# Kernel tuning notes

Measured on AMD Instinct MI355X. Metric: run time of the kernel, lower is better.

Reference implementation:

```python
import jax, jax.numpy as jnp
import numpy as np

NUM_USERS = 100000
NUM_ITEMS = 50000
EMB_DIM = 128
N_EDGES = 1600000
BATCH = 16384
L_USER = (0, 1, 2)


def setup_inputs() -> dict:
    key = jax.random.key(0)
    k1, k2, k3, k4, k5, k6 = jax.random.split(key, 6)
    users = jax.random.randint(k1, (BATCH,), 0, NUM_USERS)
    items = jax.random.randint(k2, (BATCH,), 0, NUM_ITEMS)
    edge_src = jax.random.randint(k3, (N_EDGES,), 0, NUM_USERS)
    edge_dst = jax.random.randint(k4, (N_EDGES,), 0, NUM_USERS)
    # nn.Parameter init: normal(mean=0, std=0.01)
    user_emb = jax.random.normal(k5, (NUM_USERS, EMB_DIM), dtype=jnp.float32) * 0.01
    item_emb = jax.random.normal(k6, (NUM_ITEMS, EMB_DIM), dtype=jnp.float32) * 0.01
    return {"users": users, "items": items, "edge_src": edge_src,
            "edge_dst": edge_dst, "user_emb": user_emb, "item_emb": item_emb}


def social_conv(edge_src, edge_dst, h):
    # DGL copy_u -> mean aggregation over social (user-user) edges
    msgs = h[edge_src]  # [E, D] gather
    agg = jax.ops.segment_sum(msgs, edge_dst, num_segments=NUM_USERS)  # [N, D]
    deg = jax.ops.segment_sum(jnp.ones_like(edge_dst, dtype=h.dtype), edge_dst,
                              num_segments=NUM_USERS)  # [N]
    return agg / jnp.maximum(deg, 1.0)[:, None]


def reference(users, items, edge_src, edge_dst, user_emb, item_emb):
    g1 = social_conv(edge_src, edge_dst, user_emb)
    g2 = social_conv(edge_src, edge_dst, g1)
    final_user = jnp.zeros_like(user_emb)
    if 0 in L_USER:
        final_user = final_user + user_emb
    if 1 in L_USER:
        final_user = final_user + g1
    if 2 in L_USER:
        final_user = final_user + g2
    latest_user = final_user[users]   # [B, D]
    latest_item = item_emb[items]     # [B, D]
    predict = jax.nn.sigmoid(jnp.sum(latest_user * latest_item, axis=1))  # [B]
    return predict, latest_user, latest_item
```

## Files before the change

kernel.cpp:

```cpp
#include <hip/hip_runtime.h>
#include <math.h>

#define NUM_USERS 100000
#define NUM_ITEMS 50000
#define EMB_D 128
#define N_EDGES 1600000
#define BATCH 16384

#define NBINS 782
#define CHUNK 8192
#define NCHUNKS 196
#define CELL 40
#define CAP 64

#define CVT_BLOCKS 3125

#define FP8_SCALE 512.0f
#define FP8_INV   (1.0f / 512.0f)

typedef unsigned int u32;
typedef unsigned char u8;
typedef float f32x2 __attribute__((ext_vector_type(2)));

__global__ void prep_kernel(const float* __restrict__ in, u32* __restrict__ outp,
                            const int* __restrict__ edge_src, const int* __restrict__ edge_dst,
                            u32* __restrict__ coarse, u8* __restrict__ cellcnt) {
    __shared__ int cnt2[NBINS];
    int blk = blockIdx.x;
    int tid = threadIdx.x;
    if (blk >= NCHUNKS) {
        long long bbase = (long long)(blk - NCHUNKS) * 1024;
        #pragma unroll
        for (int g = 0; g < 4; g++) {
            long long i = bbase + g * 256 + tid;
            float4 a = ((const float4*)in)[i];
            int r = __builtin_amdgcn_cvt_pk_fp8_f32(a.x * FP8_SCALE, a.y * FP8_SCALE, 0, false);
            r = __builtin_amdgcn_cvt_pk_fp8_f32(a.z * FP8_SCALE, a.w * FP8_SCALE, r, true);
            outp[i] = (u32)r;
        }
        return;
    }
    long long c0 = (long long)blk * CHUNK;
    int n = (int)min((long long)CHUNK, (long long)N_EDGES - c0);
    for (int i = tid; i < NBINS; i += 256) cnt2[i] = 0;
    __syncthreads();
    int n4 = n >> 2;
    const int4* d4p = (const int4*)(edge_dst + c0);
    const int4* s4p = (const int4*)(edge_src + c0);
    for (int i = tid; i < n4; i += 256) {
        int4 d = d4p[i];
        int4 s = s4p[i];
        int dd[4] = {d.x, d.y, d.z, d.w};
        int ss[4] = {s.x, s.y, s.z, s.w};
        #pragma unroll
        for (int k = 0; k < 4; k++) {
            int b = dd[k] >> 7;
            int idx = atomicAdd(&cnt2[b], 1);
            if (idx < CELL)
                coarse[((long long)b * NCHUNKS + blk) * CELL + idx] =
                    ((u32)ss[k] << 7) | (u32)(dd[k] & 127);
        }
    }
    __syncthreads();
    for (int i = tid; i < NBINS; i += 256)
        cellcnt[(long long)blk * NBINS + i] = (u8)min(cnt2[i], CELL);
}

__global__ void scat_kernel(const u32* __restrict__ coarse, const u8* __restrict__ cellcnt,
                            int* __restrict__ srt, int* __restrict__ counts) {
    __shared__ int cur[128];
    __shared__ __align__(16) int stage[128 * CAP];
    int b = blockIdx.x;
    int tid = threadIdx.x;
    if (tid < 128) cur[tid] = 0;
    __syncthreads();
    long long cb = (long long)b * NCHUNKS * CELL;
    for (int i = tid; i < NCHUNKS * CELL; i += 256) {
        int cell = i / CELL;
        int slot = i - cell * CELL;
        if (slot < (int)cellcnt[(long long)cell * NBINS + b]) {
            u32 p = coarse[cb + i];
            int dl = (int)(p & 127u);
            int pos = atomicAdd(&cur[dl], 1);
            if (pos < CAP) stage[(dl << 6) + pos] = (int)(p >> 7);
        }
    }
    __syncthreads();
    int binBase = b << 7;
    int rows = min(128, NUM_USERS - binBase);
    long long obase = (long long)binBase * CAP;
    int nI4 = rows << 4;
    for (int i4 = tid; i4 < nI4; i4 += 256)
        ((int4*)(srt + obase))[i4] = ((const int4*)stage)[i4];
    if (tid < 128 && tid < rows)
        counts[binBase + tid] = cur[tid];
}

__global__ void agg_kernel(const int* __restrict__ counts, const int* __restrict__ srt,
                           const u32* __restrict__ tab32, u32* __restrict__ out32) {
    int wid = (blockIdx.x * blockDim.x + threadIdx.x) >> 6;
    int lane = threadIdx.x & 63;
    if (wid >= NUM_USERS) return;
    wid = __builtin_amdgcn_readfirstlane(wid);
    int cnt = counts[wid];
    int cl = min(cnt, CAP);
    long long start = (long long)wid * CAP;
    int dlane = lane & 31;
    int hi = lane >> 5;
    float4 acc = make_float4(0.f, 0.f, 0.f, 0.f);
    int j = 0;
    for (; j + 16 <= cl; j += 16) {
        int rr[8];
        #pragma unroll
        for (int k = 0; k < 8; k++) {
            int s0 = srt[start + j + 2 * k];
            int s1 = srt[start + j + 2 * k + 1];
            rr[k] = hi ? s1 : s0;
        }
        u32 pp[8];
        #pragma unroll
        for (int k = 0; k < 8; k++) pp[k] = tab32[(long long)rr[k] * 32 + dlane];
        #pragma unroll
        for (int k = 0; k < 8; k++) {
            f32x2 d0 = __builtin_amdgcn_cvt_pk_f32_fp8((int)pp[k], false);
            f32x2 d1 = __builtin_amdgcn_cvt_pk_f32_fp8((int)pp[k], true);
            acc.x += d0.x; acc.y += d0.y; acc.z += d1.x; acc.w += d1.y;
        }
    }
    if (j < cl) {
        int rr[8]; float ww[8];
        #pragma unroll
        for (int k = 0; k < 8; k++) {
            int i0 = min(j + 2 * k, cl - 1);
            int i1 = min(j + 2 * k + 1, cl - 1);
            int s0 = srt[start + i0];
            int s1 = srt[start + i1];
            rr[k] = hi ? s1 : s0;
            ww[k] = ((j + 2 * k + hi) < cl) ? 1.0f : 0.0f;
        }
        u32 pp[8];
        #pragma unroll
        for (int k = 0; k < 8; k++) pp[k] = tab32[(long long)rr[k] * 32 + dlane];
        #pragma unroll
        for (int k = 0; k < 8; k++) {
            f32x2 d0 = __builtin_amdgcn_cvt_pk_f32_fp8((int)pp[k], false);
            f32x2 d1 = __builtin_amdgcn_cvt_pk_f32_fp8((int)pp[k], true);
            acc.x += d0.x * ww[k]; acc.y += d0.y * ww[k];
            acc.z += d1.x * ww[k]; acc.w += d1.y * ww[k];
        }
    }
    acc.x += __shfl_xor(acc.x, 32, 64);
    acc.y += __shfl_xor(acc.y, 32, 64);
    acc.z += __shfl_xor(acc.z, 32, 64);
    acc.w += __shfl_xor(acc.w, 32, 64);
    float inv = 1.0f / fmaxf((float)cnt, 1.0f);
    int enc = __builtin_amdgcn_cvt_pk_fp8_f32(acc.x * inv, acc.y * inv, 0, false);
    enc = __builtin_amdgcn_cvt_pk_fp8_f32(acc.z * inv, acc.w * inv, enc, true);
    if (lane < 32) out32[(long long)wid * 32 + dlane] = (u32)enc;
}

__global__ void final_kernel(const int* __restrict__ users, const int* __restrict__ items,
                             const float* __restrict__ user_emb, const float* __restrict__ item_emb,
                             const u32* __restrict__ g18, const int* __restrict__ counts,
                             const int* __restrict__ srt,
                             float* __restrict__ out_predict, float* __restrict__ out_lu,
                             float* __restrict__ out_li) {
    int b = (blockIdx.x * blockDim.x + threadIdx.x) >> 6;
    int lane = threadIdx.x & 63;
    if (b >= BATCH) return;
    b = __builtin_amdgcn_readfirstlane(b);
    int u = users[b];
    int it = items[b];
    int cnt = counts[u];
    int cl = min(cnt, CAP);
    long long start = (long long)u * CAP;
    int dlane = lane & 31;
    int hi = lane >> 5;
    float4 acc = make_float4(0.f, 0.f, 0.f, 0.f);
    int j = 0;
    for (; j + 16 <= cl; j += 16) {
        int rr[8];
        #pragma unroll
        for (int k = 0; k < 8; k++) {
            int s0 = srt[start + j + 2 * k];
            int s1 = srt[start + j + 2 * k + 1];
            rr[k] = hi ? s1 : s0;
        }
        u32 pp[8];
        #pragma unroll
        for (int k = 0; k < 8; k++) pp[k] = g18[(long long)rr[k] * 32 + dlane];
        #pragma unroll
        for (int k = 0; k < 8; k++) {
            f32x2 d0 = __builtin_amdgcn_cvt_pk_f32_fp8((int)pp[k], false);
            f32x2 d1 = __builtin_amdgcn_cvt_pk_f32_fp8((int)pp[k], true);
            acc.x += d0.x; acc.y += d0.y; acc.z += d1.x; acc.w += d1.y;
        }
    }
    if (j < cl) {
        int rr[8]; float ww[8];
        #pragma unroll
        for (int k = 0; k < 8; k++) {
            int i0 = min(j + 2 * k, cl - 1);
            int i1 = min(j + 2 * k + 1, cl - 1);
            int s0 = srt[start + i0];
            int s1 = srt[start + i1];
            rr[k] = hi ? s1 : s0;
            ww[k] = ((j + 2 * k + hi) < cl) ? 1.0f : 0.0f;
        }
        u32 pp[8];
        #pragma unroll
        for (int k = 0; k < 8; k++) pp[k] = g18[(long long)rr[k] * 32 + dlane];
        #pragma unroll
        for (int k = 0; k < 8; k++) {
            f32x2 d0 = __builtin_amdgcn_cvt_pk_f32_fp8((int)pp[k], false);
            f32x2 d1 = __builtin_amdgcn_cvt_pk_f32_fp8((int)pp[k], true);
            acc.x += d0.x * ww[k]; acc.y += d0.y * ww[k];
            acc.z += d1.x * ww[k]; acc.w += d1.y * ww[k];
        }
    }
    acc.x += __shfl_xor(acc.x, 32, 64);
    acc.y += __shfl_xor(acc.y, 32, 64);
    acc.z += __shfl_xor(acc.z, 32, 64);
    acc.w += __shfl_xor(acc.w, 32, 64);
    float inv = (1.0f / fmaxf((float)cnt, 1.0f)) * FP8_INV;
    float4 ue = *(const float4*)(user_emb + (long long)u * EMB_D + dlane * 4);
    u32 a1p = g18[(long long)u * 32 + dlane];
    f32x2 a0 = __builtin_amdgcn_cvt_pk_f32_fp8((int)a1p, false);
    f32x2 a1 = __builtin_amdgcn_cvt_pk_f32_fp8((int)a1p, true);
    float4 ie = *(const float4*)(item_emb + (long long)it * EMB_D + dlane * 4);
    float4 lu;
    lu.x = ue.x + a0.x * FP8_INV + acc.x * inv;
    lu.y = ue.y + a0.y * FP8_INV + acc.y * inv;
    lu.z = ue.z + a1.x * FP8_INV + acc.z * inv;
    lu.w = ue.w + a1.y * FP8_INV + acc.w * inv;
    if (lane < 32) {
        *(float4*)(out_lu + (long long)b * EMB_D + dlane * 4) = lu;
        *(float4*)(out_li + (long long)b * EMB_D + dlane * 4) = ie;
    }
    float dot = lu.x * ie.x + lu.y * ie.y + lu.z * ie.z + lu.w * ie.w;
    #pragma unroll
    for (int off = 16; off > 0; off >>= 1) dot += __shfl_down(dot, off, 64);
    if (lane == 0) out_predict[b] = 1.0f / (1.0f + expf(-dot));
}

extern "C" void kernel_launch(void* const* d_in, const int* in_sizes, int n_in,
                              void* d_out, int out_size, void* d_ws, size_t ws_size,
                              hipStream_t stream) {
    const int* users     = (const int*)d_in[0];
    const int* items     = (const int*)d_in[1];
    const int* edge_src  = (const int*)d_in[2];
    const int* edge_dst  = (const int*)d_in[3];
    const float* user_emb = (const float*)d_in[4];
    const float* item_emb = (const float*)d_in[5];

    const long long COARSE_U32 = (long long)NBINS * NCHUNKS * CELL;

    int* ws_i = (int*)d_ws;
    int* counts = ws_i;
    int* srt    = counts + 100352;
    u32* ue8    = (u32*)(srt + (long long)NUM_USERS * CAP);
    u32* coarse = ue8 + 3200000;
    u8*  cellcnt = (u8*)(coarse + COARSE_U32);
    u32* g18    = coarse;

    float* out_predict = (float*)d_out;
    float* out_lu = out_predict + BATCH;
    float* out_li = out_lu + (long long)BATCH * EMB_D;

    prep_kernel<<<NCHUNKS + CVT_BLOCKS, 256, 0, stream>>>(
        user_emb, ue8, edge_src, edge_dst, coarse, cellcnt);

    scat_kernel<<<NBINS, 256, 0, stream>>>(coarse, cellcnt, srt, counts);

    agg_kernel<<<(NUM_USERS + 3) / 4, 256, 0, stream>>>(counts, srt, ue8, g18);

    final_kernel<<<(BATCH + 3) / 4, 256, 0, stream>>>(
        users, items, user_emb, item_emb, g18, counts, srt,
        out_predict, out_lu, out_li);
}
```

Baseline: 232.4 us.

## Fuse bin scatter and first-layer aggregation into one kernel using shared-memory neighbor lists

Merges the scatter and first aggregation kernels. Each bin block now builds per-user neighbor lists in shared memory and aggregates them directly, instead of writing them to global srt and reading them back. The layer-1 result is written in place into the block's own region of the coarse buffer, and the final kernel indexes it through a new row-mapping helper. Shared-memory rows are padded to 65 entries to avoid bank conflicts, and the fp8 conversion loop now issues all its loads before converting. The trade-off is far fewer waves (782 blocks of 8 waves) for a latency-bound gather, which may lower memory-level parallelism.

```diff
diff --git a/kernel.cpp b/kernel.cpp
--- a/kernel.cpp
+++ b/kernel.cpp
@@ -12,6 +12,7 @@
 #define NCHUNKS 196
 #define CELL 40
 #define CAP 64
+#define BINSZ (NCHUNKS * CELL)
 
 #define CVT_BLOCKS 3125
 
@@ -21,6 +22,10 @@
 typedef unsigned int u32;
 typedef unsigned char u8;
 typedef float f32x2 __attribute__((ext_vector_type(2)));
+
+__device__ __forceinline__ long long g18row(int u) {
+    return (long long)(u >> 7) * BINSZ + (long long)(u & 127) * 32;
+}
 
 __global__ void prep_kernel(const float* __restrict__ in, u32* __restrict__ outp,
                             const int* __restrict__ edge_src, const int* __restrict__ edge_dst,
@@ -30,13 +35,14 @@
     int tid = threadIdx.x;
     if (blk >= NCHUNKS) {
         long long bbase = (long long)(blk - NCHUNKS) * 1024;
+        float4 a[4];
+        #pragma unroll
+        for (int g = 0; g < 4; g++) a[g] = ((const float4*)in)[bbase + g * 256 + tid];
         #pragma unroll
         for (int g = 0; g < 4; g++) {
-            long long i = bbase + g * 256 + tid;
-            float4 a = ((const float4*)in)[i];
-            int r = __builtin_amdgcn_cvt_pk_fp8_f32(a.x * FP8_SCALE, a.y * FP8_SCALE, 0, false);
-            r = __builtin_amdgcn_cvt_pk_fp8_f32(a.z * FP8_SCALE, a.w * FP8_SCALE, r, true);
-            outp[i] = (u32)r;
+            int r = __builtin_amdgcn_cvt_pk_fp8_f32(a[g].x * FP8_SCALE, a[g].y * FP8_SCALE, 0, false);
+            r = __builtin_amdgcn_cvt_pk_fp8_f32(a[g].z * FP8_SCALE, a[g].w * FP8_SCALE, r, true);
+            outp[bbase + g * 256 + tid] = (u32)r;
         }
         return;
     }
@@ -57,7 +63,7 @@
             int b = dd[k] >> 7;
             int idx = atomicAdd(&cnt2[b], 1);
             if (idx < CELL)
-                coarse[((long long)b * NCHUNKS + blk) * CELL + idx] =
+                coarse[(long long)b * BINSZ + blk * CELL + idx] =
                     ((u32)ss[k] << 7) | (u32)(dd[k] & 127);
         }
     }
@@ -66,97 +72,91 @@
         cellcnt[(long long)blk * NBINS + i] = (u8)min(cnt2[i], CELL);
 }
 
-__global__ void scat_kernel(const u32* __restrict__ coarse, const u8* __restrict__ cellcnt,
-                            int* __restrict__ srt, int* __restrict__ counts) {
+__global__ void binagg_kernel(u32* __restrict__ coarse, const u8* __restrict__ cellcnt,
+                              const u32* __restrict__ tab32,
+                              int* __restrict__ srt, int* __restrict__ counts) {
     __shared__ int cur[128];
-    __shared__ __align__(16) int stage[128 * CAP];
+    __shared__ int stage[128 * 65];
     int b = blockIdx.x;
     int tid = threadIdx.x;
     if (tid < 128) cur[tid] = 0;
     __syncthreads();
-    long long cb = (long long)b * NCHUNKS * CELL;
-    for (int i = tid; i < NCHUNKS * CELL; i += 256) {
+    long long cb = (long long)b * BINSZ;
+    for (int i = tid; i < BINSZ; i += 512) {
         int cell = i / CELL;
         int slot = i - cell * CELL;
         if (slot < (int)cellcnt[(long long)cell * NBINS + b]) {
             u32 p = coarse[cb + i];
             int dl = (int)(p & 127u);
             int pos = atomicAdd(&cur[dl], 1);
-            if (pos < CAP) stage[(dl << 6) + pos] = (int)(p >> 7);
+            if (pos < CAP) stage[dl * 65 + pos] = (int)(p >> 7);
         }
     }
     __syncthreads();
     int binBase = b << 7;
-    int rows = min(128, NUM_USERS - binBase);
-    long long obase = (long long)binBase * CAP;
-    int nI4 = rows << 4;
-    for (int i4 = tid; i4 < nI4; i4 += 256)
-        ((int4*)(srt + obase))[i4] = ((const int4*)stage)[i4];
-    if (tid < 128 && tid < rows)
-        counts[binBase + tid] = cur[tid];
-}
-
-__global__ void agg_kernel(const int* __restrict__ counts, const int* __restrict__ srt,
-                           const u32* __restrict__ tab32, u32* __restrict__ out32) {
-    int wid = (blockIdx.x * blockDim.x + threadIdx.x) >> 6;
-    int lane = threadIdx.x & 63;
-    if (wid >= NUM_USERS) return;
-    wid = __builtin_amdgcn_readfirstlane(wid);
-    int cnt = counts[wid];
-    int cl = min(cnt, CAP);
-    long long start = (long long)wid * CAP;
+    int wv = tid >> 6;
+    int lane = tid & 63;
     int dlane = lane & 31;
     int hi = lane >> 5;
-    float4 acc = make_float4(0.f, 0.f, 0.f, 0.f);
-    int j = 0;
-    for (; j + 16 <= cl; j += 16) {
-        int rr[8];
-        #pragma unroll
-        for (int k = 0; k < 8; k++) {
-            int s0 = srt[start + j + 2 * k];
-            int s1 = srt[start + j + 2 * k + 1];
-            rr[k] = hi ? s1 : s0;
-        }
-        u32 pp[8];
-        #pragma unroll
-        for (int k = 0; k < 8; k++) pp[k] = tab32[(long long)rr[k] * 32 + dlane];
-        #pragma unroll
-        for (int k = 0; k < 8; k++) {
-            f32x2 d0 = __builtin_amdgcn_cvt_pk_f32_fp8((int)pp[k], false);
-            f32x2 d1 = __builtin_amdgcn_cvt_pk_f32_fp8((int)pp[k], true);
-            acc.x += d0.x; acc.y += d0.y; acc.z += d1.x; acc.w += d1.y;
-        }
-    }
-    if (j < cl) {
-        int rr[8]; float ww[8];
-        #pragma unroll
-        for (int k = 0; k < 8; k++) {
-            int i0 = min(j + 2 * k, cl - 1);
-            int i1 = min(j + 2 * k + 1, cl - 1);
-            int s0 = srt[start + i0];
-            int s1 = srt[start + i1];
-            rr[k] = hi ? s1 : s0;
-            ww[k] = ((j + 2 * k + hi) < cl) ? 1.0f : 0.0f;
-        }
-        u32 pp[8];
-        #pragma unroll
-        for (int k = 0; k < 8; k++) pp[k] = tab32[(long long)rr[k] * 32 + dlane];
-        #pragma unroll
-        for (int k = 0; k < 8; k++) {
-            f32x2 d0 = __builtin_amdgcn_cvt_pk_f32_fp8((int)pp[k], false);
-            f32x2 d1 = __builtin_amdgcn_cvt_pk_f32_fp8((int)pp[k], true);
-            acc.x += d0.x * ww[k]; acc.y += d0.y * ww[k];
-            acc.z += d1.x * ww[k]; acc.w += d1.y * ww[k];
-        }
-    }
-    acc.x += __shfl_xor(acc.x, 32, 64);
-    acc.y += __shfl_xor(acc.y, 32, 64);
-    acc.z += __shfl_xor(acc.z, 32, 64);
-    acc.w += __shfl_xor(acc.w, 32, 64);
-    float inv = 1.0f / fmaxf((float)cnt, 1.0f);
-    int enc = __builtin_amdgcn_cvt_pk_fp8_f32(acc.x * inv, acc.y * inv, 0, false);
-    enc = __builtin_amdgcn_cvt_pk_fp8_f32(acc.z * inv, acc.w * inv, enc, true);
-    if (lane < 32) out32[(long long)wid * 32 + dlane] = (u32)enc;
+    for (int dl = wv; dl < 128; dl += 8) {
+        int user = binBase + dl;
+        if (user >= NUM_USERS) continue;
+        int cnt = cur[dl];
+        int cl = min(cnt, CAP);
+        int sbase = dl * 65;
+        float4 acc = make_float4(0.f, 0.f, 0.f, 0.f);
+        int j = 0;
+        for (; j + 16 <= cl; j += 16) {
+            int rr[8];
+            #pragma unroll
+            for (int k = 0; k < 8; k++) {
+                int s0 = stage[sbase + j + 2 * k];
+                int s1 = stage[sbase + j + 2 * k + 1];
+                rr[k] = hi ? s1 : s0;
+            }
+            u32 pp[8];
+            #pragma unroll
+            for (int k = 0; k < 8; k++) pp[k] = tab32[(long long)rr[k] * 32 + dlane];
+            #pragma unroll
+            for (int k = 0; k < 8; k++) {
+                f32x2 d0 = __builtin_amdgcn_cvt_pk_f32_fp8((int)pp[k], false);
+                f32x2 d1 = __builtin_amdgcn_cvt_pk_f32_fp8((int)pp[k], true);
+                acc.x += d0.x; acc.y += d0.y; acc.z += d1.x; acc.w += d1.y;
+            }
+        }
+        if (j < cl) {
+            int rr[8]; float ww[8];
+            #pragma unroll
+            for (int k = 0; k < 8; k++) {
+                int i0 = min(j + 2 * k, cl - 1);
+                int i1 = min(j + 2 * k + 1, cl - 1);
+                int s0 = stage[sbase + i0];
+                int s1 = stage[sbase + i1];
+                rr[k] = hi ? s1 : s0;
+                ww[k] = ((j + 2 * k + hi) < cl) ? 1.0f : 0.0f;
+            }
+            u32 pp[8];
+            #pragma unroll
+            for (int k = 0; k < 8; k++) pp[k] = tab32[(long long)rr[k] * 32 + dlane];
+            #pragma unroll
+            for (int k = 0; k < 8; k++) {
+                f32x2 d0 = __builtin_amdgcn_cvt_pk_f32_fp8((int)pp[k], false);
+                f32x2 d1 = __builtin_amdgcn_cvt_pk_f32_fp8((int)pp[k], true);
+                acc.x += d0.x * ww[k]; acc.y += d0.y * ww[k];
+                acc.z += d1.x * ww[k]; acc.w += d1.y * ww[k];
+            }
+        }
+        acc.x += __shfl_xor(acc.x, 32, 64);
+        acc.y += __shfl_xor(acc.y, 32, 64);
+        acc.z += __shfl_xor(acc.z, 32, 64);
+        acc.w += __shfl_xor(acc.w, 32, 64);
+        float inv = 1.0f / fmaxf((float)cnt, 1.0f);
+        int enc = __builtin_amdgcn_cvt_pk_fp8_f32(acc.x * inv, acc.y * inv, 0, false);
+        enc = __builtin_amdgcn_cvt_pk_fp8_f32(acc.z * inv, acc.w * inv, enc, true);
+        if (lane < 32) coarse[g18row(user) + dlane] = (u32)enc;
+        srt[(long long)user * CAP + lane] = stage[sbase + lane];
+        if (lane == 0) counts[user] = cnt;
+    }
 }
 
 __global__ void final_kernel(const int* __restrict__ users, const int* __restrict__ items,
@@ -188,7 +188,7 @@
         }
         u32 pp[8];
         #pragma unroll
-        for (int k = 0; k < 8; k++) pp[k] = g18[(long long)rr[k] * 32 + dlane];
+        for (int k = 0; k < 8; k++) pp[k] = g18[g18row(rr[k]) + dlane];
         #pragma unroll
         for (int k = 0; k < 8; k++) {
             f32x2 d0 = __builtin_amdgcn_cvt_pk_f32_fp8((int)pp[k], false);
@@ -209,7 +209,7 @@
         }
         u32 pp[8];
         #pragma unroll
-        for (int k = 0; k < 8; k++) pp[k] = g18[(long long)rr[k] * 32 + dlane];
+        for (int k = 0; k < 8; k++) pp[k] = g18[g18row(rr[k]) + dlane];
         #pragma unroll
         for (int k = 0; k < 8; k++) {
             f32x2 d0 = __builtin_amdgcn_cvt_pk_f32_fp8((int)pp[k], false);
@@ -224,7 +224,7 @@
     acc.w += __shfl_xor(acc.w, 32, 64);
     float inv = (1.0f / fmaxf((float)cnt, 1.0f)) * FP8_INV;
     float4 ue = *(const float4*)(user_emb + (long long)u * EMB_D + dlane * 4);
-    u32 a1p = g18[(long long)u * 32 + dlane];
+    u32 a1p = g18[g18row(u) + dlane];
     f32x2 a0 = __builtin_amdgcn_cvt_pk_f32_fp8((int)a1p, false);
     f32x2 a1 = __builtin_amdgcn_cvt_pk_f32_fp8((int)a1p, true);
     float4 ie = *(const float4*)(item_emb + (long long)it * EMB_D + dlane * 4);
@@ -253,7 +253,7 @@
     const float* user_emb = (const float*)d_in[4];
     const float* item_emb = (const float*)d_in[5];
 
-    const long long COARSE_U32 = (long long)NBINS * NCHUNKS * CELL;
+    const long long COARSE_U32 = (long long)NBINS * BINSZ;
 
     int* ws_i = (int*)d_ws;
     int* counts = ws_i;
@@ -261,7 +261,6 @@
     u32* ue8    = (u32*)(srt + (long long)NUM_USERS * CAP);
     u32* coarse = ue8 + 3200000;
     u8*  cellcnt = (u8*)(coarse + COARSE_U32);
-    u32* g18    = coarse;
 
     float* out_predict = (float*)d_out;
     float* out_lu = out_predict + BATCH;
@@ -270,11 +269,9 @@
     prep_kernel<<<NCHUNKS + CVT_BLOCKS, 256, 0, stream>>>(
         user_emb, ue8, edge_src, edge_dst, coarse, cellcnt);
 
-    scat_kernel<<<NBINS, 256, 0, stream>>>(coarse, cellcnt, srt, counts);
-
-    agg_kernel<<<(NUM_USERS + 3) / 4, 256, 0, stream>>>(counts, srt, ue8, g18);
+    binagg_kernel<<<NBINS, 512, 0, stream>>>(coarse, cellcnt, ue8, srt, counts);
 
     final_kernel<<<(BATCH + 3) / 4, 256, 0, stream>>>(
-        users, items, user_emb, item_emb, g18, counts, srt,
+        users, items, user_emb, item_emb, coarse, counts, srt,
         out_predict, out_lu, out_li);
 }
```

Result: no change. 232.3 us (-0.0%).
